# Kernel optimization log

Hardware: AMD Instinct MI355X
Metric: run time of the kernel (lower is better)

Reference implementation:

```python
import jax, jax.numpy as jnp
import numpy as np

N = 100000   # nodes
E = 1600000  # edges
H = 128      # hidden / feature dim
G = 64       # graphs in batch
L = 3        # GCN layers
EPS = 1e-5


def setup_inputs() -> dict:
    key = jax.random.key(0)
    ks = jax.random.split(key, 8)
    return {
        "x": jax.random.normal(ks[0], (N, H), jnp.float32),
        "edge_index": jax.random.randint(ks[1], (2, E), 0, N, dtype=jnp.int64),
        "batch": jnp.sort(jax.random.randint(ks[2], (N,), 0, G, dtype=jnp.int64)),
        "conv_w": jax.random.normal(ks[3], (L, H, H), jnp.float32) * 0.05,
        "conv_b": jnp.zeros((L, H), jnp.float32),
        "bn_g": jnp.ones((L, H), jnp.float32),
        "bn_b": jnp.zeros((L, H), jnp.float32),
        "attn_w1": jax.random.normal(ks[4], (H, H), jnp.float32) * 0.05,
        "attn_b1": jnp.zeros((H,), jnp.float32),
        "attn_w2": jax.random.normal(ks[5], (H, 1), jnp.float32) * 0.05,
        "attn_b2": jnp.zeros((1,), jnp.float32),
        "proj_w1": jax.random.normal(ks[6], (H, H), jnp.float32) * 0.05,
        "proj_b1": jnp.zeros((H,), jnp.float32),
        "proj_w2": jax.random.normal(ks[7], (H, H), jnp.float32) * 0.05,
        "proj_b2": jnp.zeros((H,), jnp.float32),
    }


def reference(x, edge_index, batch, conv_w, conv_b, bn_g, bn_b,
              attn_w1, attn_b1, attn_w2, attn_b2,
              proj_w1, proj_b1, proj_w2, proj_b2):
    n = x.shape[0]
    # GCNConv normalization: add self-loops, norm = d^-1/2[src] * d^-1/2[dst]
    loops = jnp.arange(n)
    src = jnp.concatenate([edge_index[0], loops])
    dst = jnp.concatenate([edge_index[1], loops])
    deg = jax.ops.segment_sum(jnp.ones_like(src, dtype=x.dtype), dst, num_segments=n)
    dinv = jax.lax.rsqrt(deg)  # deg >= 1 due to self-loops
    norm = (dinv[src] * dinv[dst])[:, None]  # [E+N, 1]

    h = x
    for i in range(L):
        identity = h
        z = h @ conv_w[i]                                          # [N, H]
        agg = jax.ops.segment_sum(z[src] * norm, dst, num_segments=n) + conv_b[i]
        # BatchNorm1d (training: batch statistics, biased variance)
        mean = jnp.mean(agg, axis=0)
        var = jnp.mean(jnp.square(agg - mean), axis=0)
        z = (agg - mean) * jax.lax.rsqrt(var + EPS) * bn_g[i] + bn_b[i]
        z = jax.nn.relu(z)
        if i > 0:
            z = z + identity
        h = z

    # Graph attention: softmax over all nodes (dim=0), elementwise reweight
    a = jnp.tanh(h @ attn_w1 + attn_b1) @ attn_w2 + attn_b2        # [N, 1]
    a = jax.nn.softmax(a, axis=0)
    h = h * a

    # global_mean_pool over batch ids
    sums = jax.ops.segment_sum(h, batch, num_segments=G)           # [G, H]
    counts = jax.ops.segment_sum(jnp.ones((n, 1), x.dtype), batch, num_segments=G)
    pooled = sums / jnp.maximum(counts, 1.0)

    # projection MLP
    out = jax.nn.relu(pooled @ proj_w1 + proj_b1) @ proj_w2 + proj_b2
    return out
```

## Files before the change

### kernel.cpp

```cpp
#include <hip/hip_runtime.h>

#define HH 128
#define GG 64
#define EPS 1e-5f

__device__ __forceinline__ unsigned femax_enc(float f) {
    unsigned u = __float_as_uint(f);
    return (u & 0x80000000u) ? ~u : (u | 0x80000000u);
}
__device__ __forceinline__ float femax_dec(unsigned u) {
    return (u & 0x80000000u) ? __uint_as_float(u & 0x7FFFFFFFu) : __uint_as_float(~u);
}

__global__ void k_count(const int* __restrict__ dst, int* __restrict__ cnt, int E) {
    int i = blockIdx.x * blockDim.x + threadIdx.x;
    if (i < E) atomicAdd(&cnt[dst[i]], 1);
}

__global__ __launch_bounds__(512) void k_scanA(const int* __restrict__ cnt, int* __restrict__ tmp,
                                               int* __restrict__ bsum, int n) {
    __shared__ int s[512];
    int t = threadIdx.x;
    int i = blockIdx.x * 512 + t;
    s[t] = (i < n) ? cnt[i] : 0;
    __syncthreads();
    for (int o = 1; o < 512; o <<= 1) {
        int u = (t >= o) ? s[t - o] : 0;
        __syncthreads();
        s[t] += u;
        __syncthreads();
    }
    if (i < n) tmp[i] = s[t];
    if (t == 511) bsum[blockIdx.x] = s[511];
}

__global__ __launch_bounds__(512) void k_scanB(int* __restrict__ bsum, int nb) {
    __shared__ int s[512];
    int t = threadIdx.x;
    s[t] = (t < nb) ? bsum[t] : 0;
    __syncthreads();
    for (int o = 1; o < 512; o <<= 1) {
        int u = (t >= o) ? s[t - o] : 0;
        __syncthreads();
        s[t] += u;
        __syncthreads();
    }
    if (t < nb) bsum[t] = s[t];
}

__global__ void k_scanC(const int* __restrict__ tmp, const int* __restrict__ bsum,
                        const int* __restrict__ cnt, int* __restrict__ rowptr,
                        float* __restrict__ dinv, int n) {
    int i = blockIdx.x * blockDim.x + threadIdx.x;
    if (i < n) {
        int b = i >> 9;
        int off = (b > 0) ? bsum[b - 1] : 0;
        rowptr[i + 1] = tmp[i] + off;
        if (i == 0) rowptr[0] = 0;
        dinv[i] = rsqrtf((float)(cnt[i] + 1));
    }
}

__global__ void k_fill(const int* __restrict__ src, const int* __restrict__ dst,
                       const int* __restrict__ rowptr, int* __restrict__ cursor,
                       const float* __restrict__ dinv, int2* __restrict__ epk, int E) {
    int e = blockIdx.x * blockDim.x + threadIdx.x;
    if (e < E) {
        int s0 = src[e], d0 = dst[e];
        int p = atomicAdd(&cursor[d0], 1);
        int idx = rowptr[d0] + p;
        epk[idx] = make_int2(s0, __float_as_int(dinv[s0] * dinv[d0]));
    }
}

#define FMA_ROW(i, a)                       \
    acc[i][0] = fmaf(a, w0.x, acc[i][0]);   \
    acc[i][1] = fmaf(a, w0.y, acc[i][1]);   \
    acc[i][2] = fmaf(a, w0.z, acc[i][2]);   \
    acc[i][3] = fmaf(a, w0.w, acc[i][3]);   \
    acc[i][4] = fmaf(a, w1.x, acc[i][4]);   \
    acc[i][5] = fmaf(a, w1.y, acc[i][5]);   \
    acc[i][6] = fmaf(a, w1.z, acc[i][6]);   \
    acc[i][7] = fmaf(a, w1.w, acc[i][7]);

template <int BNIN, int ACT>
__global__ __launch_bounds__(256, 3) void k_gemm(const float* __restrict__ Ain, float* __restrict__ Aio,
                                                 const float* __restrict__ res,
                                                 const float* __restrict__ csum, const float* __restrict__ csq,
                                                 const float* __restrict__ bng, const float* __restrict__ bnb,
                                                 const float* __restrict__ W, const float* __restrict__ bias,
                                                 float* __restrict__ C, const float* __restrict__ w2,
                                                 const float* __restrict__ b2, unsigned* __restrict__ gmax,
                                                 int n) {
    __shared__ float hl[64][132];
    __shared__ float Ws[32][128];
    int tb = blockIdx.x * 64;
    int t = threadIdx.x;
    int rows = n - tb; if (rows > 64) rows = 64;
    int c4 = (t & 31) << 2;

    float A0c = 0.f, A1c = 0.f, A2c = 0.f, A3c = 0.f;
    float B0c = 0.f, B1c = 0.f, B2c = 0.f, B3c = 0.f;
    if (BNIN) {
        float4 cs = *(const float4*)&csum[c4];
        float4 cq = *(const float4*)&csq[c4];
        float4 gg = *(const float4*)&bng[c4];
        float4 bb = *(const float4*)&bnb[c4];
        float inv_n = 1.0f / (float)n;
        float m0 = cs.x * inv_n, m1 = cs.y * inv_n, m2 = cs.z * inv_n, m3 = cs.w * inv_n;
        A0c = rsqrtf(cq.x * inv_n - m0 * m0 + EPS) * gg.x;
        A1c = rsqrtf(cq.y * inv_n - m1 * m1 + EPS) * gg.y;
        A2c = rsqrtf(cq.z * inv_n - m2 * m2 + EPS) * gg.z;
        A3c = rsqrtf(cq.w * inv_n - m3 * m3 + EPS) * gg.w;
        B0c = bb.x - m0 * A0c; B1c = bb.y - m1 * A1c; B2c = bb.z - m2 * A2c; B3c = bb.w - m3 * A3c;
    }
    for (int idx = t; idx < 64 * 32; idx += 256) {
        int r = idx >> 5;
        if (r < rows) {
            size_t go = (size_t)(tb + r) * HH + c4;
            float4 v = *(const float4*)&Ain[go];
            if (BNIN) {
                v.x = fmaxf(fmaf(v.x, A0c, B0c), 0.f);
                v.y = fmaxf(fmaf(v.y, A1c, B1c), 0.f);
                v.z = fmaxf(fmaf(v.z, A2c, B2c), 0.f);
                v.w = fmaxf(fmaf(v.w, A3c, B3c), 0.f);
                if (res) {
                    float4 rv = *(const float4*)&res[go];
                    v.x += rv.x; v.y += rv.y; v.z += rv.z; v.w += rv.w;
                }
                *(float4*)&Aio[go] = v;
            }
            *(float4*)&hl[r][c4] = v;
        }
    }
    int tx = t & 15;
    int ty = t >> 4;
    int tx8 = tx << 3;
    float acc[4][8] = {};
    for (int kc = 0; kc < 4; ++kc) {
        __syncthreads();
        for (int idx = t; idx < 32 * 32; idx += 256) {
            int r = idx >> 5, cc4 = (idx & 31) << 2;
            *(float4*)&Ws[r][cc4] = *(const float4*)&W[(size_t)(kc * 32 + r) * HH + cc4];
        }
        __syncthreads();
        int kb = kc * 32;
        for (int k = 0; k < 32; ++k) {
            float4 w0 = *(const float4*)&Ws[k][tx8];
            float4 w1 = *(const float4*)&Ws[k][tx8 + 4];
            float a0 = hl[ty][kb + k];
            float a1 = hl[ty + 16][kb + k];
            float a2 = hl[ty + 32][kb + k];
            float a3 = hl[ty + 48][kb + k];
            FMA_ROW(0, a0)
            FMA_ROW(1, a1)
            FMA_ROW(2, a2)
            FMA_ROW(3, a3)
        }
    }
    if (ACT == 0) {
#pragma unroll
        for (int i = 0; i < 4; ++i) {
            int r = tb + ty + 16 * i;
            if (r < n) {
                float4 o0 = {acc[i][0], acc[i][1], acc[i][2], acc[i][3]};
                float4 o1 = {acc[i][4], acc[i][5], acc[i][6], acc[i][7]};
                *(float4*)&C[(size_t)r * HH + tx8] = o0;
                *(float4*)&C[(size_t)r * HH + tx8 + 4] = o1;
            }
        }
    } else {
        float b1v[8], w2v[8];
#pragma unroll
        for (int j = 0; j < 8; ++j) { b1v[j] = bias[tx8 + j]; w2v[j] = w2[tx8 + j]; }
        float b2s = b2[0];
        float lmax = -3.4e38f;
#pragma unroll
        for (int i = 0; i < 4; ++i) {
            float s = 0.f;
#pragma unroll
            for (int j = 0; j < 8; ++j)
                s = fmaf(tanhf(acc[i][j] + b1v[j]), w2v[j], s);
            s += __shfl_xor(s, 1);
            s += __shfl_xor(s, 2);
            s += __shfl_xor(s, 4);
            s += __shfl_xor(s, 8);
            int r = tb + ty + 16 * i;
            float val = s + b2s;
            if (r < n) {
                lmax = fmaxf(lmax, val);
                if (tx == 0) C[r] = val;
            }
        }
        lmax = fmaxf(lmax, __shfl_xor(lmax, 16));
        lmax = fmaxf(lmax, __shfl_xor(lmax, 32));
        __shared__ float wm[4];
        if ((t & 63) == 0) wm[t >> 6] = lmax;
        __syncthreads();
        if (t == 0) {
            float m = fmaxf(fmaxf(wm[0], wm[1]), fmaxf(wm[2], wm[3]));
            atomicMax(gmax, femax_enc(m));
        }
    }
}

#define AGG_FMA(vv, ww)                                           \
    acc.x = fmaf(vv.x, ww, acc.x); acc.y = fmaf(vv.y, ww, acc.y); \
    acc.z = fmaf(vv.z, ww, acc.z); acc.w = fmaf(vv.w, ww, acc.w);

__global__ __launch_bounds__(256) void k_agg(const float* __restrict__ z, const int* __restrict__ rowptr,
                                             const int2* __restrict__ epk, const float* __restrict__ dinv,
                                             const float* __restrict__ bias, float* __restrict__ agg, int n) {
    int wid = (int)((blockIdx.x * (size_t)blockDim.x + threadIdx.x) >> 6);
    if (wid >= n) return;
    int lane = threadIdx.x & 63;
    int half = lane >> 5;
    int c0 = (lane & 31) << 2;
    int beg = rowptr[wid], end = rowptr[wid + 1];
    float4 acc = {0.f, 0.f, 0.f, 0.f};
    if (half == 0) {
        float di = dinv[wid];
        float ws = di * di;
        float4 zs = *(const float4*)&z[(size_t)wid * HH + c0];
        acc.x = zs.x * ws; acc.y = zs.y * ws; acc.z = zs.z * ws; acc.w = zs.w * ws;
    }
    for (int e = beg + half; e < end; e += 16) {
        int2 p[8];
        float w[8];
#pragma unroll
        for (int j = 0; j < 8; ++j) {
            int idx = e + 2 * j;
            bool valid = idx < end;
            p[j] = epk[valid ? idx : beg];
            w[j] = valid ? __int_as_float(p[j].y) : 0.f;
        }
        float4 v[8];
#pragma unroll
        for (int j = 0; j < 8; ++j)
            v[j] = *(const float4*)&z[(size_t)p[j].x * HH + c0];
#pragma unroll
        for (int j = 0; j < 8; ++j) { AGG_FMA(v[j], w[j]) }
    }
    acc.x += __shfl_xor(acc.x, 32);
    acc.y += __shfl_xor(acc.y, 32);
    acc.z += __shfl_xor(acc.z, 32);
    acc.w += __shfl_xor(acc.w, 32);
    if (half == 0) {
        float4 b4 = *(const float4*)&bias[c0];
        acc.x += b4.x; acc.y += b4.y; acc.z += b4.z; acc.w += b4.w;
        *(float4*)&agg[(size_t)wid * HH + c0] = acc;
    }
}

__global__ __launch_bounds__(256) void k_bnstats(const float* __restrict__ agg, float* __restrict__ colsum,
                                                 float* __restrict__ colsq, int n) {
    int t = threadIdx.x;
    int col = t & 127, sub = t >> 7;
    int rpb = (n + gridDim.x - 1) / gridDim.x;
    int r0 = blockIdx.x * rpb;
    int r1 = r0 + rpb; if (r1 > n) r1 = n;
    float s = 0.f, q = 0.f;
    for (int r = r0 + sub; r < r1; r += 2) {
        float v = agg[(size_t)r * HH + col];
        s += v;
        q = fmaf(v, v, q);
    }
    __shared__ float ls[256], lq[256];
    ls[t] = s; lq[t] = q;
    __syncthreads();
    if (t < 128) {
        atomicAdd(&colsum[col], ls[t] + ls[t + 128]);
        atomicAdd(&colsq[col], lq[t] + lq[t + 128]);
    }
}

__global__ __launch_bounds__(256) void k_pool(const float* __restrict__ h, const float* __restrict__ apre,
                                              const int* __restrict__ batch, const unsigned* __restrict__ gmax,
                                              float* __restrict__ pooled, float* __restrict__ counts,
                                              float* __restrict__ Sglob, int n) {
    float M = femax_dec(*gmax);
    int t = threadIdx.x;
    int col = t & 127, sub = t >> 7;
    int rpb = (n + gridDim.x - 1) / gridDim.x;
    int r0 = blockIdx.x * rpb;
    int r1 = r0 + rpb; if (r1 > n) r1 = n;
    float acc = 0.f, cntf = 0.f, es = 0.f;
    int cur = -1;
    for (int r = r0 + sub; r < r1; r += 2) {
        int g = batch[r];
        if (g != cur) {
            if (cur >= 0) {
                atomicAdd(&pooled[cur * HH + col], acc);
                if (col == 0) atomicAdd(&counts[cur], cntf);
            }
            cur = g; acc = 0.f; cntf = 0.f;
        }
        float s = expf(apre[r] - M);
        acc = fmaf(h[(size_t)r * HH + col], s, acc);
        cntf += 1.0f;
        if (col == 0) es += s;
    }
    if (cur >= 0) {
        atomicAdd(&pooled[cur * HH + col], acc);
        if (col == 0) atomicAdd(&counts[cur], cntf);
    }
    if (col == 0 && es != 0.f) atomicAdd(Sglob, es);
}

__global__ __launch_bounds__(128) void k_mlp(const float* __restrict__ pooled, const float* __restrict__ counts,
                                             const float* __restrict__ Sglob, const float* __restrict__ W1,
                                             const float* __restrict__ b1, const float* __restrict__ W2,
                                             const float* __restrict__ b2, float* __restrict__ out) {
    int g = blockIdx.x;
    int t = threadIdx.x;
    __shared__ float p[128], t1[128];
    float S = Sglob[0];
    float c = fmaxf(counts[g], 1.0f);
    p[t] = pooled[g * HH + t] / (S * c);
    __syncthreads();
    float acc = b1[t];
    for (int k = 0; k < 128; ++k) acc = fmaf(p[k], W1[k * HH + t], acc);
    t1[t] = fmaxf(acc, 0.f);
    __syncthreads();
    float acc2 = b2[t];
    for (int j = 0; j < 128; ++j) acc2 = fmaf(t1[j], W2[j * HH + t], acc2);
    out[g * HH + t] = acc2;
}

extern "C" void kernel_launch(void* const* d_in, const int* in_sizes, int n_in,
                              void* d_out, int out_size, void* d_ws, size_t ws_size,
                              hipStream_t stream) {
    const float* x       = (const float*)d_in[0];
    const int*   ei      = (const int*)d_in[1];
    const int*   batch   = (const int*)d_in[2];
    const float* conv_w  = (const float*)d_in[3];
    const float* conv_b  = (const float*)d_in[4];
    const float* bn_g    = (const float*)d_in[5];
    const float* bn_b    = (const float*)d_in[6];
    const float* attn_w1 = (const float*)d_in[7];
    const float* attn_b1 = (const float*)d_in[8];
    const float* attn_w2 = (const float*)d_in[9];
    const float* attn_b2 = (const float*)d_in[10];
    const float* proj_w1 = (const float*)d_in[11];
    const float* proj_b1 = (const float*)d_in[12];
    const float* proj_w2 = (const float*)d_in[13];
    const float* proj_b2 = (const float*)d_in[14];

    const int E = in_sizes[1] / 2;
    const int n = in_sizes[2];
    const int* srcp = ei;
    const int* dstp = ei + E;

    char* base = (char*)d_ws;
    size_t off = 0;
    auto alloc = [&](size_t bytes) -> char* {
        char* p = base + off;
        off = (off + bytes + 511) & ~(size_t)511;
        return p;
    };
    int*   cntcur  = (int*)alloc((size_t)2 * n * 4);
    int*   cnt     = cntcur;
    int*   cursor  = cntcur + n;
    int*   rowptr  = (int*)alloc((size_t)(n + 1) * 4);
    int*   tmp     = (int*)alloc((size_t)n * 4);
    int*   bsum    = (int*)alloc(512 * 4);
    float* dinv    = (float*)alloc((size_t)n * 4);
    int2*  epk     = (int2*)alloc((size_t)E * 8);
    float* z       = (float*)alloc((size_t)n * HH * 4);
    float* aggA    = (float*)alloc((size_t)n * HH * 4);
    float* aggB    = (float*)alloc((size_t)n * HH * 4);
    float* apre    = (float*)alloc((size_t)n * 4);
    float* zarena  = (float*)alloc((size_t)(1024 + GG * HH + GG) * 4);
    float* cs0 = zarena;            float* cq0 = zarena + 128;
    float* cs1 = zarena + 256;      float* cq1 = zarena + 384;
    float* cs2 = zarena + 512;      float* cq2 = zarena + 640;
    unsigned* gmaxu = (unsigned*)(zarena + 768);
    float* Sglob  = zarena + 769;
    float* pooled = zarena + 1024;
    float* counts = zarena + 1024 + GG * HH;
    const size_t zbytes = (size_t)(1024 + GG * HH + GG) * 4;

    const int eGrid    = (E + 255) / 256;
    const int nGrid    = (n + 255) / 256;
    const int nbScan   = (n + 511) / 512;
    const int gemmGrid = (n + 63) / 64;
    const int waveGrid = (n + 3) / 4;

    hipMemsetAsync(zarena, 0, zbytes, stream);
    hipMemsetAsync(cntcur, 0, (size_t)2 * n * 4, stream);
    k_count<<<eGrid, 256, 0, stream>>>(dstp, cnt, E);
    k_scanA<<<nbScan, 512, 0, stream>>>(cnt, tmp, bsum, n);
    k_scanB<<<1, 512, 0, stream>>>(bsum, nbScan);
    k_scanC<<<nGrid, 256, 0, stream>>>(tmp, bsum, cnt, rowptr, dinv, n);
    k_fill<<<eGrid, 256, 0, stream>>>(srcp, dstp, rowptr, cursor, dinv, epk, E);

    k_gemm<0, 0><<<gemmGrid, 256, 0, stream>>>(x, nullptr, nullptr, nullptr, nullptr, nullptr, nullptr,
                                               conv_w, nullptr, z, nullptr, nullptr, nullptr, n);
    k_agg<<<waveGrid, 256, 0, stream>>>(z, rowptr, epk, dinv, conv_b, aggA, n);
    k_bnstats<<<1024, 256, 0, stream>>>(aggA, cs0, cq0, n);

    k_gemm<1, 0><<<gemmGrid, 256, 0, stream>>>(aggA, aggA, nullptr, cs0, cq0, bn_g, bn_b,
                                               conv_w + (size_t)HH * HH, nullptr, z, nullptr, nullptr,
                                               nullptr, n);
    k_agg<<<waveGrid, 256, 0, stream>>>(z, rowptr, epk, dinv, conv_b + HH, aggB, n);
    k_bnstats<<<1024, 256, 0, stream>>>(aggB, cs1, cq1, n);

    k_gemm<1, 0><<<gemmGrid, 256, 0, stream>>>(aggB, aggB, aggA, cs1, cq1, bn_g + HH, bn_b + HH,
                                               conv_w + (size_t)2 * HH * HH, nullptr, z, nullptr, nullptr,
                                               nullptr, n);
    k_agg<<<waveGrid, 256, 0, stream>>>(z, rowptr, epk, dinv, conv_b + 2 * HH, aggA, n);
    k_bnstats<<<1024, 256, 0, stream>>>(aggA, cs2, cq2, n);

    k_gemm<1, 1><<<gemmGrid, 256, 0, stream>>>(aggA, aggA, aggB, cs2, cq2, bn_g + 2 * HH, bn_b + 2 * HH,
                                               attn_w1, attn_b1, apre, attn_w2, attn_b2, gmaxu, n);

    k_pool<<<1024, 256, 0, stream>>>(aggA, apre, batch, gmaxu, pooled, counts, Sglob, n);
    k_mlp<<<GG, 128, 0, stream>>>(pooled, counts, Sglob, proj_w1, proj_b1, proj_w2, proj_b2,
                                  (float*)d_out);
}
```

Before: 1.081 ms.

## Double-buffer GEMM weight tiles with register prefetch and strided column mapping

The dense GEMM kernel now streams the weight matrix in 16-row chunks through a two-slot shared buffer. The next chunk is prefetched into registers while the current one is consumed, which removes one of the two barriers per chunk and hides global load latency. The A operand is read as float4 across k, and each thread's output columns change from 8 contiguous to a stride of 16, which changes the LDS access pattern and makes output stores scalar but coalesced across threads. The cost is more registers for the prefetch and unrolled inner loops, which could reduce occupancy.

```diff
diff --git a/kernel.cpp b/kernel.cpp
--- a/kernel.cpp
+++ b/kernel.cpp
@@ -73,16 +73,6 @@
     }
 }
 
-#define FMA_ROW(i, a)                       \
-    acc[i][0] = fmaf(a, w0.x, acc[i][0]);   \
-    acc[i][1] = fmaf(a, w0.y, acc[i][1]);   \
-    acc[i][2] = fmaf(a, w0.z, acc[i][2]);   \
-    acc[i][3] = fmaf(a, w0.w, acc[i][3]);   \
-    acc[i][4] = fmaf(a, w1.x, acc[i][4]);   \
-    acc[i][5] = fmaf(a, w1.y, acc[i][5]);   \
-    acc[i][6] = fmaf(a, w1.z, acc[i][6]);   \
-    acc[i][7] = fmaf(a, w1.w, acc[i][7]);
-
 template <int BNIN, int ACT>
 __global__ __launch_bounds__(256, 3) void k_gemm(const float* __restrict__ Ain, float* __restrict__ Aio,
                                                  const float* __restrict__ res,
@@ -93,11 +83,12 @@
                                                  const float* __restrict__ b2, unsigned* __restrict__ gmax,
                                                  int n) {
     __shared__ float hl[64][132];
-    __shared__ float Ws[32][128];
+    __shared__ float Ws[2][16][128];
     int tb = blockIdx.x * 64;
     int t = threadIdx.x;
     int rows = n - tb; if (rows > 64) rows = 64;
     int c4 = (t & 31) << 2;
+    int wr = t >> 5;
 
     float A0c = 0.f, A1c = 0.f, A2c = 0.f, A3c = 0.f;
     float B0c = 0.f, B1c = 0.f, B2c = 0.f, B3c = 0.f;
@@ -114,6 +105,9 @@
         A3c = rsqrtf(cq.w * inv_n - m3 * m3 + EPS) * gg.w;
         B0c = bb.x - m0 * A0c; B1c = bb.y - m1 * A1c; B2c = bb.z - m2 * A2c; B3c = bb.w - m3 * A3c;
     }
+    float4 wp0 = *(const float4*)&W[(size_t)wr * HH + c4];
+    float4 wp1 = *(const float4*)&W[(size_t)(wr + 8) * HH + c4];
+
     for (int idx = t; idx < 64 * 32; idx += 256) {
         int r = idx >> 5;
         if (r < rows) {
@@ -133,29 +127,44 @@
             *(float4*)&hl[r][c4] = v;
         }
     }
+    *(float4*)&Ws[0][wr][c4] = wp0;
+    *(float4*)&Ws[0][wr + 8][c4] = wp1;
+
     int tx = t & 15;
     int ty = t >> 4;
-    int tx8 = tx << 3;
     float acc[4][8] = {};
-    for (int kc = 0; kc < 4; ++kc) {
-        __syncthreads();
-        for (int idx = t; idx < 32 * 32; idx += 256) {
-            int r = idx >> 5, cc4 = (idx & 31) << 2;
-            *(float4*)&Ws[r][cc4] = *(const float4*)&W[(size_t)(kc * 32 + r) * HH + cc4];
-        }
-        __syncthreads();
-        int kb = kc * 32;
-        for (int k = 0; k < 32; ++k) {
-            float4 w0 = *(const float4*)&Ws[k][tx8];
-            float4 w1 = *(const float4*)&Ws[k][tx8 + 4];
-            float a0 = hl[ty][kb + k];
-            float a1 = hl[ty + 16][kb + k];
-            float a2 = hl[ty + 32][kb + k];
-            float a3 = hl[ty + 48][kb + k];
-            FMA_ROW(0, a0)
-            FMA_ROW(1, a1)
-            FMA_ROW(2, a2)
-            FMA_ROW(3, a3)
+    for (int kc = 0; kc < 8; ++kc) {
+        if (kc < 7) {
+            wp0 = *(const float4*)&W[(size_t)((kc + 1) * 16 + wr) * HH + c4];
+            wp1 = *(const float4*)&W[(size_t)((kc + 1) * 16 + wr + 8) * HH + c4];
+        }
+        __syncthreads();
+        const float (*Wc)[128] = Ws[kc & 1];
+        int kb = kc * 16;
+#pragma unroll
+        for (int k4 = 0; k4 < 16; k4 += 4) {
+            float a0v[4], a1v[4], a2v[4], a3v[4];
+            *(float4*)a0v = *(const float4*)&hl[ty][kb + k4];
+            *(float4*)a1v = *(const float4*)&hl[ty + 16][kb + k4];
+            *(float4*)a2v = *(const float4*)&hl[ty + 32][kb + k4];
+            *(float4*)a3v = *(const float4*)&hl[ty + 48][kb + k4];
+#pragma unroll
+            for (int j = 0; j < 4; ++j) {
+                float wv[8];
+#pragma unroll
+                for (int c = 0; c < 8; ++c) wv[c] = Wc[k4 + j][tx + 16 * c];
+#pragma unroll
+                for (int c = 0; c < 8; ++c) {
+                    acc[0][c] = fmaf(a0v[j], wv[c], acc[0][c]);
+                    acc[1][c] = fmaf(a1v[j], wv[c], acc[1][c]);
+                    acc[2][c] = fmaf(a2v[j], wv[c], acc[2][c]);
+                    acc[3][c] = fmaf(a3v[j], wv[c], acc[3][c]);
+                }
+            }
+        }
+        if (kc < 7) {
+            *(float4*)&Ws[(kc + 1) & 1][wr][c4] = wp0;
+            *(float4*)&Ws[(kc + 1) & 1][wr + 8][c4] = wp1;
         }
     }
     if (ACT == 0) {
@@ -163,16 +172,15 @@
         for (int i = 0; i < 4; ++i) {
             int r = tb + ty + 16 * i;
             if (r < n) {
-                float4 o0 = {acc[i][0], acc[i][1], acc[i][2], acc[i][3]};
-                float4 o1 = {acc[i][4], acc[i][5], acc[i][6], acc[i][7]};
-                *(float4*)&C[(size_t)r * HH + tx8] = o0;
-                *(float4*)&C[(size_t)r * HH + tx8 + 4] = o1;
+#pragma unroll
+                for (int c = 0; c < 8; ++c)
+                    C[(size_t)r * HH + tx + 16 * c] = acc[i][c];
             }
         }
     } else {
         float b1v[8], w2v[8];
 #pragma unroll
-        for (int j = 0; j < 8; ++j) { b1v[j] = bias[tx8 + j]; w2v[j] = w2[tx8 + j]; }
+        for (int j = 0; j < 8; ++j) { b1v[j] = bias[tx + 16 * j]; w2v[j] = w2[tx + 16 * j]; }
         float b2s = b2[0];
         float lmax = -3.4e38f;
 #pragma unroll
```

Result: slower. 1.424 ms (+31.8%).

## Make dense GEMM persistent with resident weights and double-buffered input tiles

Applied to the files above, without the earlier changes.

The node-feature GEMM becomes a persistent kernel: 256 blocks each load the whole 128x128 weight matrix into LDS once, then stride over 64-row tiles. The next tile is prefetched into registers and staged into a double-buffered LDS area while the current tile is multiplied. The inner loop now reads A as float4 and uses a split column mapping (ca/cb). The goal is to stop reloading W for every tile and to hide global-load latency. The cost is about 135KB of LDS per block, so only one block (four waves) fits per CU, which may limit memory-level parallelism.

```diff
diff --git a/kernel.cpp b/kernel.cpp
--- a/kernel.cpp
+++ b/kernel.cpp
@@ -83,8 +83,14 @@
     acc[i][6] = fmaf(a, w1.z, acc[i][6]);   \
     acc[i][7] = fmaf(a, w1.w, acc[i][7]);
 
+#define QUAD(kk, a0e, a1e, a2e, a3e) {                  \
+    float4 w0 = *(const float4*)&Wl[k + kk][ca];        \
+    float4 w1 = *(const float4*)&Wl[k + kk][cb];        \
+    FMA_ROW(0, a0e) FMA_ROW(1, a1e)                     \
+    FMA_ROW(2, a2e) FMA_ROW(3, a3e) }
+
 template <int BNIN, int ACT>
-__global__ __launch_bounds__(256, 3) void k_gemm(const float* __restrict__ Ain, float* __restrict__ Aio,
+__global__ __launch_bounds__(256, 1) void k_gemm(const float* __restrict__ Ain, float* __restrict__ Aio,
                                                  const float* __restrict__ res,
                                                  const float* __restrict__ csum, const float* __restrict__ csq,
                                                  const float* __restrict__ bng, const float* __restrict__ bnb,
@@ -92,12 +98,16 @@
                                                  float* __restrict__ C, const float* __restrict__ w2,
                                                  const float* __restrict__ b2, unsigned* __restrict__ gmax,
                                                  int n) {
-    __shared__ float hl[64][132];
-    __shared__ float Ws[32][128];
-    int tb = blockIdx.x * 64;
-    int t = threadIdx.x;
-    int rows = n - tb; if (rows > 64) rows = 64;
+    __shared__ float Wl[128][132];
+    __shared__ float Ab[2][64][132];
+    __shared__ float wm[4];
+    int t = threadIdx.x;
+    int tx = t & 15, ty = t >> 4;
+    int ca = tx << 2;
+    int cb = 64 + (tx << 2);
     int c4 = (t & 31) << 2;
+    int sr = t >> 5;
+    int ntiles = (n + 63) >> 6;
 
     float A0c = 0.f, A1c = 0.f, A2c = 0.f, A3c = 0.f;
     float B0c = 0.f, B1c = 0.f, B2c = 0.f, B3c = 0.f;
@@ -114,93 +124,125 @@
         A3c = rsqrtf(cq.w * inv_n - m3 * m3 + EPS) * gg.w;
         B0c = bb.x - m0 * A0c; B1c = bb.y - m1 * A1c; B2c = bb.z - m2 * A2c; B3c = bb.w - m3 * A3c;
     }
-    for (int idx = t; idx < 64 * 32; idx += 256) {
-        int r = idx >> 5;
-        if (r < rows) {
-            size_t go = (size_t)(tb + r) * HH + c4;
-            float4 v = *(const float4*)&Ain[go];
-            if (BNIN) {
-                v.x = fmaxf(fmaf(v.x, A0c, B0c), 0.f);
-                v.y = fmaxf(fmaf(v.y, A1c, B1c), 0.f);
-                v.z = fmaxf(fmaf(v.z, A2c, B2c), 0.f);
-                v.w = fmaxf(fmaf(v.w, A3c, B3c), 0.f);
-                if (res) {
-                    float4 rv = *(const float4*)&res[go];
-                    v.x += rv.x; v.y += rv.y; v.z += rv.z; v.w += rv.w;
+
+#pragma unroll
+    for (int i = 0; i < 16; ++i) {
+        int r = sr + (i << 3);
+        *(float4*)&Wl[r][c4] = *(const float4*)&W[(size_t)r * HH + c4];
+    }
+
+    float4 aR[8], rR[8];
+    int tile = blockIdx.x;
+    if (tile < ntiles) {
+        int tb = tile << 6;
+        int rows = n - tb; if (rows > 64) rows = 64;
+#pragma unroll
+        for (int j = 0; j < 8; ++j) {
+            int r = sr + (j << 3);
+            if (r < rows) {
+                size_t go = (size_t)(tb + r) * HH + c4;
+                aR[j] = *(const float4*)&Ain[go];
+                if (BNIN && res) rR[j] = *(const float4*)&res[go];
+            }
+        }
+    }
+    int cur = 0;
+    for (; tile < ntiles; tile += gridDim.x) {
+        int tb = tile << 6;
+        int rows = n - tb; if (rows > 64) rows = 64;
+#pragma unroll
+        for (int j = 0; j < 8; ++j) {
+            int r = sr + (j << 3);
+            if (r < rows) {
+                float4 v = aR[j];
+                if (BNIN) {
+                    v.x = fmaxf(fmaf(v.x, A0c, B0c), 0.f);
+                    v.y = fmaxf(fmaf(v.y, A1c, B1c), 0.f);
+                    v.z = fmaxf(fmaf(v.z, A2c, B2c), 0.f);
+                    v.w = fmaxf(fmaf(v.w, A3c, B3c), 0.f);
+                    if (res) {
+                        float4 rv = rR[j];
+                        v.x += rv.x; v.y += rv.y; v.z += rv.z; v.w += rv.w;
+                    }
+                    *(float4*)&Aio[(size_t)(tb + r) * HH + c4] = v;
                 }
-                *(float4*)&Aio[go] = v;
-            }
-            *(float4*)&hl[r][c4] = v;
-        }
-    }
-    int tx = t & 15;
-    int ty = t >> 4;
-    int tx8 = tx << 3;
-    float acc[4][8] = {};
-    for (int kc = 0; kc < 4; ++kc) {
+                *(float4*)&Ab[cur][r][c4] = v;
+            }
+        }
+        int nxt = tile + gridDim.x;
+        if (nxt < ntiles) {
+            int tb2 = nxt << 6;
+            int rows2 = n - tb2; if (rows2 > 64) rows2 = 64;
+#pragma unroll
+            for (int j = 0; j < 8; ++j) {
+                int r = sr + (j << 3);
+                if (r < rows2) {
+                    size_t go = (size_t)(tb2 + r) * HH + c4;
+                    aR[j] = *(const float4*)&Ain[go];
+                    if (BNIN && res) rR[j] = *(const float4*)&res[go];
+                }
+            }
+        }
         __syncthreads();
-        for (int idx = t; idx < 32 * 32; idx += 256) {
-            int r = idx >> 5, cc4 = (idx & 31) << 2;
-            *(float4*)&Ws[r][cc4] = *(const float4*)&W[(size_t)(kc * 32 + r) * HH + cc4];
-        }
-        __syncthreads();
-        int kb = kc * 32;
-        for (int k = 0; k < 32; ++k) {
-            float4 w0 = *(const float4*)&Ws[k][tx8];
-            float4 w1 = *(const float4*)&Ws[k][tx8 + 4];
-            float a0 = hl[ty][kb + k];
-            float a1 = hl[ty + 16][kb + k];
-            float a2 = hl[ty + 32][kb + k];
-            float a3 = hl[ty + 48][kb + k];
-            FMA_ROW(0, a0)
-            FMA_ROW(1, a1)
-            FMA_ROW(2, a2)
-            FMA_ROW(3, a3)
-        }
-    }
-    if (ACT == 0) {
-#pragma unroll
-        for (int i = 0; i < 4; ++i) {
-            int r = tb + ty + 16 * i;
-            if (r < n) {
-                float4 o0 = {acc[i][0], acc[i][1], acc[i][2], acc[i][3]};
-                float4 o1 = {acc[i][4], acc[i][5], acc[i][6], acc[i][7]};
-                *(float4*)&C[(size_t)r * HH + tx8] = o0;
-                *(float4*)&C[(size_t)r * HH + tx8 + 4] = o1;
-            }
-        }
-    } else {
-        float b1v[8], w2v[8];
-#pragma unroll
-        for (int j = 0; j < 8; ++j) { b1v[j] = bias[tx8 + j]; w2v[j] = w2[tx8 + j]; }
-        float b2s = b2[0];
-        float lmax = -3.4e38f;
-#pragma unroll
-        for (int i = 0; i < 4; ++i) {
-            float s = 0.f;
-#pragma unroll
-            for (int j = 0; j < 8; ++j)
-                s = fmaf(tanhf(acc[i][j] + b1v[j]), w2v[j], s);
-            s += __shfl_xor(s, 1);
-            s += __shfl_xor(s, 2);
-            s += __shfl_xor(s, 4);
-            s += __shfl_xor(s, 8);
-            int r = tb + ty + 16 * i;
-            float val = s + b2s;
-            if (r < n) {
-                lmax = fmaxf(lmax, val);
-                if (tx == 0) C[r] = val;
-            }
-        }
-        lmax = fmaxf(lmax, __shfl_xor(lmax, 16));
-        lmax = fmaxf(lmax, __shfl_xor(lmax, 32));
-        __shared__ float wm[4];
-        if ((t & 63) == 0) wm[t >> 6] = lmax;
-        __syncthreads();
-        if (t == 0) {
-            float m = fmaxf(fmaxf(wm[0], wm[1]), fmaxf(wm[2], wm[3]));
-            atomicMax(gmax, femax_enc(m));
-        }
+        float acc[4][8] = {};
+#pragma unroll 4
+        for (int k = 0; k < 128; k += 4) {
+            float4 a0 = *(const float4*)&Ab[cur][ty][k];
+            float4 a1 = *(const float4*)&Ab[cur][ty + 16][k];
+            float4 a2 = *(const float4*)&Ab[cur][ty + 32][k];
+            float4 a3 = *(const float4*)&Ab[cur][ty + 48][k];
+            QUAD(0, a0.x, a1.x, a2.x, a3.x)
+            QUAD(1, a0.y, a1.y, a2.y, a3.y)
+            QUAD(2, a0.z, a1.z, a2.z, a3.z)
+            QUAD(3, a0.w, a1.w, a2.w, a3.w)
+        }
+        if (ACT == 0) {
+#pragma unroll
+            for (int i = 0; i < 4; ++i) {
+                int r = tb + ty + (i << 4);
+                if (r < n) {
+                    float4 o0 = {acc[i][0], acc[i][1], acc[i][2], acc[i][3]};
+                    float4 o1 = {acc[i][4], acc[i][5], acc[i][6], acc[i][7]};
+                    *(float4*)&C[(size_t)r * HH + ca] = o0;
+                    *(float4*)&C[(size_t)r * HH + cb] = o1;
+                }
+            }
+        } else {
+            float b1v[8], w2v[8];
+#pragma unroll
+            for (int j = 0; j < 4; ++j) {
+                b1v[j] = bias[ca + j];     w2v[j] = w2[ca + j];
+                b1v[4 + j] = bias[cb + j]; w2v[4 + j] = w2[cb + j];
+            }
+            float b2s = b2[0];
+            float lmax = -3.4e38f;
+#pragma unroll
+            for (int i = 0; i < 4; ++i) {
+                float s = 0.f;
+#pragma unroll
+                for (int j = 0; j < 8; ++j)
+                    s = fmaf(tanhf(acc[i][j] + b1v[j]), w2v[j], s);
+                s += __shfl_xor(s, 1);
+                s += __shfl_xor(s, 2);
+                s += __shfl_xor(s, 4);
+                s += __shfl_xor(s, 8);
+                int r = tb + ty + (i << 4);
+                float val = s + b2s;
+                if (r < n) {
+                    lmax = fmaxf(lmax, val);
+                    if (tx == 0) C[r] = val;
+                }
+            }
+            lmax = fmaxf(lmax, __shfl_xor(lmax, 16));
+            lmax = fmaxf(lmax, __shfl_xor(lmax, 32));
+            if ((t & 63) == 0) wm[t >> 6] = lmax;
+            __syncthreads();
+            if (t == 0) {
+                float m = fmaxf(fmaxf(wm[0], wm[1]), fmaxf(wm[2], wm[3]));
+                atomicMax(gmax, femax_enc(m));
+            }
+        }
+        cur ^= 1;
     }
 }
 
@@ -383,7 +425,6 @@
     const int eGrid    = (E + 255) / 256;
     const int nGrid    = (n + 255) / 256;
     const int nbScan   = (n + 511) / 512;
-    const int gemmGrid = (n + 63) / 64;
     const int waveGrid = (n + 3) / 4;
 
     hipMemsetAsync(zarena, 0, zbytes, stream);
@@ -394,25 +435,25 @@
     k_scanC<<<nGrid, 256, 0, stream>>>(tmp, bsum, cnt, rowptr, dinv, n);
     k_fill<<<eGrid, 256, 0, stream>>>(srcp, dstp, rowptr, cursor, dinv, epk, E);
 
-    k_gemm<0, 0><<<gemmGrid, 256, 0, stream>>>(x, nullptr, nullptr, nullptr, nullptr, nullptr, nullptr,
-                                               conv_w, nullptr, z, nullptr, nullptr, nullptr, n);
+    k_gemm<0, 0><<<256, 256, 0, stream>>>(x, nullptr, nullptr, nullptr, nullptr, nullptr, nullptr,
+                                          conv_w, nullptr, z, nullptr, nullptr, nullptr, n);
     k_agg<<<waveGrid, 256, 0, stream>>>(z, rowptr, epk, dinv, conv_b, aggA, n);
     k_bnstats<<<1024, 256, 0, stream>>>(aggA, cs0, cq0, n);
 
-    k_gemm<1, 0><<<gemmGrid, 256, 0, stream>>>(aggA, aggA, nullptr, cs0, cq0, bn_g, bn_b,
-                                               conv_w + (size_t)HH * HH, nullptr, z, nullptr, nullptr,
-                                               nullptr, n);
+    k_gemm<1, 0><<<256, 256, 0, stream>>>(aggA, aggA, nullptr, cs0, cq0, bn_g, bn_b,
+                                          conv_w + (size_t)HH * HH, nullptr, z, nullptr, nullptr,
+                                          nullptr, n);
     k_agg<<<waveGrid, 256, 0, stream>>>(z, rowptr, epk, dinv, conv_b + HH, aggB, n);
     k_bnstats<<<1024, 256, 0, stream>>>(aggB, cs1, cq1, n);
 
-    k_gemm<1, 0><<<gemmGrid, 256, 0, stream>>>(aggB, aggB, aggA, cs1, cq1, bn_g + HH, bn_b + HH,
-                                               conv_w + (size_t)2 * HH * HH, nullptr, z, nullptr, nullptr,
-                                               nullptr, n);
+    k_gemm<1, 0><<<256, 256, 0, stream>>>(aggB, aggB, aggA, cs1, cq1, bn_g + HH, bn_b + HH,
+                                          conv_w + (size_t)2 * HH * HH, nullptr, z, nullptr, nullptr,
+                                          nullptr, n);
     k_agg<<<waveGrid, 256, 0, stream>>>(z, rowptr, epk, dinv, conv_b + 2 * HH, aggA, n);
     k_bnstats<<<1024, 256, 0, stream>>>(aggA, cs2, cq2, n);
 
-    k_gemm<1, 1><<<gemmGrid, 256, 0, stream>>>(aggA, aggA, aggB, cs2, cq2, bn_g + 2 * HH, bn_b + 2 * HH,
-                                               attn_w1, attn_b1, apre, attn_w2, attn_b2, gmaxu, n);
+    k_gemm<1, 1><<<256, 256, 0, stream>>>(aggA, aggA, aggB, cs2, cq2, bn_g + 2 * HH, bn_b + 2 * HH,
+                                          attn_w1, attn_b1, apre, attn_w2, attn_b2, gmaxu, n);
 
     k_pool<<<1024, 256, 0, stream>>>(aggA, apre, batch, gmaxu, pooled, counts, Sglob, n);
     k_mlp<<<GG, 128, 0, stream>>>(pooled, counts, Sglob, proj_w1, proj_b1, proj_w2, proj_b2,
```

Result: slower. 1.124 ms (+4.0%).
